# Kernel optimization log

Measured on AMD Instinct MI355X. Metric: run time of the kernel, lower is better.

The kernel has to match this reference:

```python
import jax, jax.numpy as jnp
import numpy as np

N_NODES, N_EDGES, F_DIM, H_DIM = 50000, 800000, 128, 128
BN_EPS = 1e-3  # keras BatchNormalization default epsilon


def setup_inputs() -> dict:
    key = jax.random.key(0)
    k0, k1, k2 = jax.random.split(key, 3)
    edge_pairs = jax.random.randint(k0, (N_EDGES, 2), 0, N_NODES, dtype=jnp.int64 if jax.config.jax_enable_x64 else jnp.int32)
    node_features = jax.random.normal(k1, (N_NODES, F_DIM), dtype=jnp.float32)
    W = jax.random.normal(k2, (F_DIM, H_DIM), dtype=jnp.float32) * (1.0 / np.sqrt(F_DIM))
    b = jnp.zeros((H_DIM,), jnp.float32)
    gamma = jnp.ones((H_DIM,), jnp.float32)
    beta = jnp.zeros((H_DIM,), jnp.float32)
    moving_mean = jnp.zeros((H_DIM,), jnp.float32)
    moving_var = jnp.ones((H_DIM,), jnp.float32)
    return {"edge_pairs": edge_pairs, "node_features": node_features, "W": W, "b": b,
            "gamma": gamma, "beta": beta, "moving_mean": moving_mean, "moving_var": moving_var}


def reference(edge_pairs, node_features, W, b, gamma, beta, moving_mean, moving_var):
    src = edge_pairs[:, 0]
    dst = edge_pairs[:, 1]
    n = node_features.shape[0]

    # linear transform (dropout inactive: training=False)
    t = node_features @ W + b  # [N, H]

    # out-degree by source node
    deg = jax.ops.segment_sum(jnp.ones(src.shape[0], t.dtype), src, num_segments=n)  # [N]
    inv_sqrt_deg = jnp.power(deg, -0.5)  # matches tf.pow(d, -0.5)

    # degree-normalized neighbour messages: d_src^-1/2 * d_dst^-1/2 * t[dst]
    scale = (inv_sqrt_deg[src] * inv_sqrt_deg[dst])[:, None]  # [E,1]
    nb_sum = jax.ops.segment_sum(t[dst] * scale, src, num_segments=n)  # [N, H]

    # source term: segment_mean(deg[src] * t[src]) ; empty segments -> 0 (tf semantics)
    msg = deg[src][:, None] * t[src]  # [E, H]
    seg = jax.ops.segment_sum(msg, src, num_segments=n)  # [N, H]
    src_mean = jnp.where(deg[:, None] > 0, seg / jnp.maximum(deg, 1.0)[:, None], 0.0)

    agg = 0.5 * nb_sum + 0.5 * src_mean

    # batchnorm, inference mode (moving statistics)
    return (agg - moving_mean) * jax.lax.rsqrt(moving_var + BN_EPS) * gamma + beta
```

## Files before the change

kernel.cpp:

```cpp
#include <hip/hip_runtime.h>
#include <math.h>

#define BN_EPS 0.001f
#define CHUNK 2048
#define MAXBUCK 1024

typedef __attribute__((ext_vector_type(8))) short bf16x8;
typedef __attribute__((ext_vector_type(4))) float f32x4;
typedef __attribute__((ext_vector_type(2))) float f32x2;

__device__ inline unsigned bf16rne(float f) {
  unsigned u = __float_as_uint(f);
  return (u + 0x7fffu + ((u >> 16) & 1u)) >> 16;
}

__global__ __launch_bounds__(256) void k_ehist(const int2* __restrict__ ep, int ne,
                                               int nbuck, int* __restrict__ ghist) {
  __shared__ int h[MAXBUCK];
  int c = blockIdx.x, t = threadIdx.x;
  for (int i = t; i < nbuck; i += 256) h[i] = 0;
  __syncthreads();
  int base = c * CHUNK;
  int end = min(base + CHUNK, ne);
  for (int e = base + t; e < end; e += 256) atomicAdd(&h[ep[e].x >> 6], 1);
  __syncthreads();
  int* row = ghist + (size_t)c * nbuck;
  for (int i = t; i < nbuck; i += 256) row[i] = h[i];
}

__global__ __launch_bounds__(512) void k_bscan(int* __restrict__ ghist, int nchunk,
                                               int nbuck, int* __restrict__ btot) {
  __shared__ int s0[512], s1[512];
  int b = blockIdx.x, t = threadIdx.x;
  int v = (t < nchunk) ? ghist[(size_t)t * nbuck + b] : 0;
  s0[t] = v;
  __syncthreads();
  int* src = s0; int* dst = s1;
  for (int off = 1; off < 512; off <<= 1) {
    int x = src[t];
    if (t >= off) x += src[t - off];
    dst[t] = x;
    __syncthreads();
    int* tmp = src; src = dst; dst = tmp;
  }
  if (t < nchunk) ghist[(size_t)t * nbuck + b] = src[t] - v;
  if (t == 0) btot[b] = src[511];
}

__global__ __launch_bounds__(1024) void k_bbase(const int* __restrict__ btot, int nbuck,
                                                int* __restrict__ bbase) {
  __shared__ int s0[1024], s1[1024];
  int t = threadIdx.x;
  int v = (t < nbuck) ? btot[t] : 0;
  s0[t] = v;
  __syncthreads();
  int* src = s0; int* dst = s1;
  for (int off = 1; off < 1024; off <<= 1) {
    int x = src[t];
    if (t >= off) x += src[t - off];
    dst[t] = x;
    __syncthreads();
    int* tmp = src; src = dst; dst = tmp;
  }
  if (t < nbuck) bbase[t] = src[t] - v;
}

__global__ __launch_bounds__(256) void k_ebin(const int2* __restrict__ ep, int ne,
                                              int nbuck, const int* __restrict__ ghist,
                                              const int* __restrict__ bbase,
                                              unsigned* __restrict__ bins) {
  __shared__ int cur[MAXBUCK];
  int c = blockIdx.x, t = threadIdx.x;
  const int* row = ghist + (size_t)c * nbuck;
  for (int i = t; i < nbuck; i += 256) cur[i] = bbase[i] + row[i];
  __syncthreads();
  int base = c * CHUNK;
  int end = min(base + CHUNK, ne);
  for (int e = base + t; e < end; e += 256) {
    int2 p = ep[e];
    int pos = atomicAdd(&cur[p.x >> 6], 1);
    bins[pos] = (unsigned)p.y | ((unsigned)(p.x & 63) << 17);
  }
}

__global__ __launch_bounds__(256) void k_bfinal(const int* __restrict__ bbase,
                                                const int* __restrict__ btot,
                                                const unsigned* __restrict__ bins,
                                                int n, int* __restrict__ deg,
                                                float* __restrict__ isd,
                                                int* __restrict__ offsets,
                                                int* __restrict__ csr_dst) {
  __shared__ int h[64];
  __shared__ int cur[64];
  int bk = blockIdx.x, t = threadIdx.x;
  if (t < 64) h[t] = 0;
  __syncthreads();
  int s = bbase[bk], cnt = btot[bk];
  for (int i = t; i < cnt; i += 256) atomicAdd(&h[bins[s + i] >> 17], 1);
  __syncthreads();
  if (t == 0) {
    int run = s;
    for (int j = 0; j < 64; ++j) { cur[j] = run; run += h[j]; }
  }
  __syncthreads();
  if (t < 64) {
    int node = (bk << 6) + t;
    if (node < n) {
      deg[node] = h[t];
      offsets[node] = cur[t];
      isd[node] = 1.0f / sqrtf((float)h[t]);
    }
  }
  __syncthreads();
  for (int i = t; i < cnt; i += 256) {
    unsigned r = bins[s + i];
    int pos = atomicAdd(&cur[r >> 17], 1);
    csr_dst[pos] = (int)(r & 0x1FFFFu);
  }
}

__global__ __launch_bounds__(256) void k_wsplit(const float* __restrict__ W,
                                                unsigned short* __restrict__ Wh,
                                                unsigned short* __restrict__ Wl) {
  int g = blockIdx.x * 256 + threadIdx.x;
  int frag = g >> 6;
  int lane = g & 63;
  int ct = frag >> 2, ks = frag & 3;
  int col = ct * 16 + (lane & 15);
  int k0 = ks * 32 + (lane >> 4) * 8;
  unsigned short h8[8], l8[8];
#pragma unroll
  for (int j = 0; j < 8; ++j) {
    float x = W[(size_t)(k0 + j) * 128 + col];
    unsigned short h = (unsigned short)(__float_as_uint(x) >> 16);
    float rem = x - __uint_as_float((unsigned)h << 16);
    h8[j] = h;
    l8[j] = (unsigned short)bf16rne(rem);
  }
  *(uint4*)&Wh[(size_t)frag * 512 + lane * 8] = *(uint4*)h8;
  *(uint4*)&Wl[(size_t)frag * 512 + lane * 8] = *(uint4*)l8;
}

__global__ __launch_bounds__(256, 4) void k_gemm(const float* __restrict__ X,
                                                 const unsigned short* __restrict__ Wh,
                                                 const unsigned short* __restrict__ Wl,
                                                 const float* __restrict__ b,
                                                 const float* __restrict__ isd,
                                                 float* __restrict__ T,
                                                 unsigned char* __restrict__ Tb8, int M) {
  int tid = threadIdx.x;
  int wave = tid >> 6, lane = tid & 63;
  int r16 = lane & 15, kq = lane >> 4;
  int ch = wave & 1;
  int rowbase = blockIdx.x * 32 + (wave >> 1) * 16;
  int arow = rowbase + r16;
  bool aok = arow < M;
  const float* xr = X + ((size_t)arow << 7);

  bf16x8 ah[4], al[4];
#pragma unroll
  for (int ks = 0; ks < 4; ++ks) {
    int k0 = ks * 32 + kq * 8;
    float4 v0 = aok ? *(const float4*)(xr + k0) : make_float4(0.f, 0.f, 0.f, 0.f);
    float4 v1 = aok ? *(const float4*)(xr + k0 + 4) : make_float4(0.f, 0.f, 0.f, 0.f);
    float f[8] = {v0.x, v0.y, v0.z, v0.w, v1.x, v1.y, v1.z, v1.w};
    bf16x8 h8, l8;
#pragma unroll
    for (int j = 0; j < 8; ++j) {
      unsigned short h = (unsigned short)(__float_as_uint(f[j]) >> 16);
      float rem = f[j] - __uint_as_float((unsigned)h << 16);
      h8[j] = (short)h;
      l8[j] = (short)bf16rne(rem);
    }
    ah[ks] = h8;
    al[ks] = l8;
  }

  f32x4 acc[4] = {};
#pragma unroll
  for (int ks = 0; ks < 4; ++ks) {
#pragma unroll
    for (int ct = 0; ct < 4; ++ct) {
      int frag = (ch * 4 + ct) * 4 + ks;
      bf16x8 bh = *(const bf16x8*)&Wh[(size_t)frag * 512 + lane * 8];
      bf16x8 bl = *(const bf16x8*)&Wl[(size_t)frag * 512 + lane * 8];
      acc[ct] = __builtin_amdgcn_mfma_f32_16x16x32_bf16(ah[ks], bh, acc[ct], 0, 0, 0);
      acc[ct] = __builtin_amdgcn_mfma_f32_16x16x32_bf16(ah[ks], bl, acc[ct], 0, 0, 0);
      acc[ct] = __builtin_amdgcn_mfma_f32_16x16x32_bf16(al[ks], bh, acc[ct], 0, 0, 0);
    }
  }

  float bias[4];
#pragma unroll
  for (int ct = 0; ct < 4; ++ct) bias[ct] = b[(ch * 4 + ct) * 16 + r16];
  int orow[4];
  float isdr[4];
#pragma unroll
  for (int r = 0; r < 4; ++r) {
    orow[r] = rowbase + kq * 4 + r;
    isdr[r] = (orow[r] < M) ? isd[orow[r]] : 0.f;
  }
#pragma unroll
  for (int ct = 0; ct < 4; ++ct) {
    int col = (ch * 4 + ct) * 16 + r16;
#pragma unroll
    for (int r = 0; r < 4; ++r) {
      float v = acc[ct][r] + bias[ct];
      bool ok = orow[r] < M;
      if (ok) T[((size_t)orow[r] << 7) + col] = v;
      float sv = v * isdr[r];
      float other = __shfl_xor(sv, 1);
      int pk01 = __builtin_amdgcn_cvt_pk_fp8_f32(sv, other, 0, false);
      int pk23 = __shfl_xor(pk01, 2);
      if (ok && (r16 & 3) == 0) {
        unsigned dword = ((unsigned)pk01 & 0xFFFFu) | ((unsigned)pk23 << 16);
        *(unsigned*)&Tb8[((size_t)orow[r] << 7) + (ch * 4 + ct) * 16 + r16] = dword;
      }
    }
  }
}

__global__ __launch_bounds__(256) void k_gather(
    const float* __restrict__ T, const unsigned char* __restrict__ Tb8,
    const int* __restrict__ deg, const float* __restrict__ isd,
    const int* __restrict__ offsets, const int* __restrict__ csr_dst,
    const float* __restrict__ mm, const float* __restrict__ var,
    const float* __restrict__ gamma, const float* __restrict__ beta,
    float* __restrict__ out, int n, int ne) {
  int wave = threadIdx.x >> 6;
  int lane = threadIdx.x & 63;
  int i = blockIdx.x * 4 + wave;
  if (i >= n) return;
  int degi = deg[i];
  int start = offsets[i];
  const unsigned short* rows = (const unsigned short*)Tb8;
  float sx[16] = {}, sy[16] = {};
  for (int e = 0; e < degi; e += 16) {
    int ii = start + e + (lane & 15);
    int dv = (ii < ne) ? csr_dst[ii] : 0;
    unsigned short r[16];
#pragma unroll
    for (int j = 0; j < 16; ++j) {
      int idx = __shfl(dv, j);
      r[j] = rows[((size_t)idx << 6) + lane];
    }
#pragma unroll
    for (int j = 0; j < 16; ++j) {
      int rr = (e + j < degi) ? (int)r[j] : 0;
      f32x2 f = __builtin_amdgcn_cvt_pk_f32_fp8(rr, false);
      sx[j] += f.x;
      sy[j] += f.y;
    }
  }
  float fx = (((sx[0] + sx[1]) + (sx[2] + sx[3])) + ((sx[4] + sx[5]) + (sx[6] + sx[7]))) +
             (((sx[8] + sx[9]) + (sx[10] + sx[11])) + ((sx[12] + sx[13]) + (sx[14] + sx[15])));
  float fy = (((sy[0] + sy[1]) + (sy[2] + sy[3])) + ((sy[4] + sy[5]) + (sy[6] + sy[7]))) +
             (((sy[8] + sy[9]) + (sy[10] + sy[11])) + ((sy[12] + sy[13]) + (sy[14] + sy[15])));
  float aggx = 0.f, aggy = 0.f;
  if (degi > 0) {
    float2 tv = ((const float2*)(T + ((size_t)i << 7)))[lane];
    float isi = isd[i];
    float di = (float)degi;
    aggx = 0.5f * (isi * fx) + 0.5f * (di * tv.x);
    aggy = 0.5f * (isi * fy) + 0.5f * (di * tv.y);
  }
  float2 mmv = ((const float2*)mm)[lane];
  float2 vv = ((const float2*)var)[lane];
  float2 gv = ((const float2*)gamma)[lane];
  float2 bv = ((const float2*)beta)[lane];
  float2 res;
  res.x = (aggx - mmv.x) * rsqrtf(vv.x + BN_EPS) * gv.x + bv.x;
  res.y = (aggy - mmv.y) * rsqrtf(vv.y + BN_EPS) * gv.y + bv.y;
  ((float2*)(out + ((size_t)i << 7)))[lane] = res;
}

static inline size_t align_up(size_t x) { return (x + 255) & ~(size_t)255; }

extern "C" void kernel_launch(void* const* d_in, const int* in_sizes, int n_in,
                              void* d_out, int out_size, void* d_ws, size_t ws_size,
                              hipStream_t stream) {
  const int2* ep = (const int2*)d_in[0];
  const float* X = (const float*)d_in[1];
  const float* W = (const float*)d_in[2];
  const float* b = (const float*)d_in[3];
  const float* gamma = (const float*)d_in[4];
  const float* beta = (const float*)d_in[5];
  const float* mm = (const float*)d_in[6];
  const float* var = (const float*)d_in[7];
  float* out = (float*)d_out;

  const int ne = in_sizes[0] / 2;
  const int n = in_sizes[1] / 128;
  const int nbuck = (n + 63) >> 6;
  const int nchunk = (ne + CHUNK - 1) / CHUNK;

  char* p = (char*)d_ws;
  int* deg = (int*)p;        p += align_up((size_t)n * 4);
  float* isd = (float*)p;    p += align_up((size_t)n * 4);
  int* offsets = (int*)p;    p += align_up((size_t)n * 4);
  int* btot = (int*)p;       p += align_up((size_t)nbuck * 4);
  int* bbase = (int*)p;      p += align_up((size_t)nbuck * 4);
  int* ghist = (int*)p;      p += align_up((size_t)nchunk * nbuck * 4);
  int* csr_dst = (int*)p;    p += align_up((size_t)ne * 4);
  unsigned* bins = (unsigned*)p; p += align_up((size_t)ne * 4);
  unsigned short* Wh = (unsigned short*)p; p += align_up((size_t)128 * 128 * 2);
  unsigned short* Wl = (unsigned short*)p; p += align_up((size_t)128 * 128 * 2);
  float* T = (float*)p;      p += align_up((size_t)n * 128 * 4);
  unsigned char* Tb8 = (unsigned char*)p; p += align_up((size_t)n * 128);

  k_ehist<<<nchunk, 256, 0, stream>>>(ep, ne, nbuck, ghist);
  k_bscan<<<nbuck, 512, 0, stream>>>(ghist, nchunk, nbuck, btot);
  k_bbase<<<1, 1024, 0, stream>>>(btot, nbuck, bbase);
  k_ebin<<<nchunk, 256, 0, stream>>>(ep, ne, nbuck, ghist, bbase, bins);
  k_bfinal<<<nbuck, 256, 0, stream>>>(bbase, btot, bins, n, deg, isd, offsets, csr_dst);
  k_wsplit<<<8, 256, 0, stream>>>(W, Wh, Wl);
  k_gemm<<<(n + 31) / 32, 256, 0, stream>>>(X, Wh, Wl, b, isd, T, Tb8, n);
  k_gather<<<(n + 3) / 4, 256, 0, stream>>>(T, Tb8, deg, isd, offsets, csr_dst,
                                            mm, var, gamma, beta, out, n, ne);
}
```

Baseline: 96.13 us.

## Fuse W bf16 split into GEMM via LDS staging with 1024-thread blocks

Removes the separate k_wsplit launch. Each GEMM block now loads W from global memory, splits it into bf16 hi/lo parts and stores them in LDS in MFMA fragment order. Blocks grow to 1024 threads covering 256 rows, and each wave computes all 128 output columns instead of half. This saves one kernel launch and the global Wh/Wl buffers. In exchange every block redoes the W conversion, uses 64KB of LDS, and runs only 196 blocks, which may limit occupancy.

```diff
diff --git a/kernel.cpp b/kernel.cpp
--- a/kernel.cpp
+++ b/kernel.cpp
@@ -119,40 +119,40 @@
   }
 }
 
-__global__ __launch_bounds__(256) void k_wsplit(const float* __restrict__ W,
-                                                unsigned short* __restrict__ Wh,
-                                                unsigned short* __restrict__ Wl) {
-  int g = blockIdx.x * 256 + threadIdx.x;
-  int frag = g >> 6;
-  int lane = g & 63;
-  int ct = frag >> 2, ks = frag & 3;
-  int col = ct * 16 + (lane & 15);
-  int k0 = ks * 32 + (lane >> 4) * 8;
-  unsigned short h8[8], l8[8];
-#pragma unroll
-  for (int j = 0; j < 8; ++j) {
-    float x = W[(size_t)(k0 + j) * 128 + col];
-    unsigned short h = (unsigned short)(__float_as_uint(x) >> 16);
-    float rem = x - __uint_as_float((unsigned)h << 16);
-    h8[j] = h;
-    l8[j] = (unsigned short)bf16rne(rem);
-  }
-  *(uint4*)&Wh[(size_t)frag * 512 + lane * 8] = *(uint4*)h8;
-  *(uint4*)&Wl[(size_t)frag * 512 + lane * 8] = *(uint4*)l8;
-}
-
-__global__ __launch_bounds__(256, 4) void k_gemm(const float* __restrict__ X,
-                                                 const unsigned short* __restrict__ Wh,
-                                                 const unsigned short* __restrict__ Wl,
-                                                 const float* __restrict__ b,
-                                                 const float* __restrict__ isd,
-                                                 float* __restrict__ T,
-                                                 unsigned char* __restrict__ Tb8, int M) {
+__global__ __launch_bounds__(1024, 4) void k_gemm(const float* __restrict__ X,
+                                                  const float* __restrict__ W,
+                                                  const float* __restrict__ b,
+                                                  const float* __restrict__ isd,
+                                                  float* __restrict__ T,
+                                                  unsigned char* __restrict__ Tb8, int M) {
+  __shared__ unsigned short WhL[16384];
+  __shared__ unsigned short WlL[16384];
   int tid = threadIdx.x;
+
+#pragma unroll
+  for (int it = 0; it < 4; ++it) {
+    int q = tid + it * 1024;
+    int k = q >> 5;
+    int c0 = (q & 31) * 4;
+    float4 v = ((const float4*)W)[q];
+    float vv[4] = {v.x, v.y, v.z, v.w};
+#pragma unroll
+    for (int j2 = 0; j2 < 4; ++j2) {
+      int col = c0 + j2;
+      float x = vv[j2];
+      unsigned short hh = (unsigned short)(__float_as_uint(x) >> 16);
+      float rem = x - __uint_as_float((unsigned)hh << 16);
+      int frag = ((col >> 4) << 2) | (k >> 5);
+      int ln = (((k >> 3) & 3) << 4) | (col & 15);
+      int addr = frag * 512 + ln * 8 + (k & 7);
+      WhL[addr] = hh;
+      WlL[addr] = (unsigned short)bf16rne(rem);
+    }
+  }
+
   int wave = tid >> 6, lane = tid & 63;
   int r16 = lane & 15, kq = lane >> 4;
-  int ch = wave & 1;
-  int rowbase = blockIdx.x * 32 + (wave >> 1) * 16;
+  int rowbase = blockIdx.x * 256 + wave * 16;
   int arow = rowbase + r16;
   bool aok = arow < M;
   const float* xr = X + ((size_t)arow << 7);
@@ -167,32 +167,30 @@
     bf16x8 h8, l8;
 #pragma unroll
     for (int j = 0; j < 8; ++j) {
-      unsigned short h = (unsigned short)(__float_as_uint(f[j]) >> 16);
-      float rem = f[j] - __uint_as_float((unsigned)h << 16);
-      h8[j] = (short)h;
+      unsigned short hh = (unsigned short)(__float_as_uint(f[j]) >> 16);
+      float rem = f[j] - __uint_as_float((unsigned)hh << 16);
+      h8[j] = (short)hh;
       l8[j] = (short)bf16rne(rem);
     }
     ah[ks] = h8;
     al[ks] = l8;
   }
-
-  f32x4 acc[4] = {};
-#pragma unroll
-  for (int ks = 0; ks < 4; ++ks) {
-#pragma unroll
-    for (int ct = 0; ct < 4; ++ct) {
-      int frag = (ch * 4 + ct) * 4 + ks;
-      bf16x8 bh = *(const bf16x8*)&Wh[(size_t)frag * 512 + lane * 8];
-      bf16x8 bl = *(const bf16x8*)&Wl[(size_t)frag * 512 + lane * 8];
+  __syncthreads();
+
+  f32x4 acc[8] = {};
+#pragma unroll
+  for (int ct = 0; ct < 8; ++ct) {
+#pragma unroll
+    for (int ks = 0; ks < 4; ++ks) {
+      int base = (ct * 4 + ks) * 512 + lane * 8;
+      bf16x8 bh = *(const bf16x8*)&WhL[base];
+      bf16x8 bl = *(const bf16x8*)&WlL[base];
       acc[ct] = __builtin_amdgcn_mfma_f32_16x16x32_bf16(ah[ks], bh, acc[ct], 0, 0, 0);
       acc[ct] = __builtin_amdgcn_mfma_f32_16x16x32_bf16(ah[ks], bl, acc[ct], 0, 0, 0);
       acc[ct] = __builtin_amdgcn_mfma_f32_16x16x32_bf16(al[ks], bh, acc[ct], 0, 0, 0);
     }
   }
 
-  float bias[4];
-#pragma unroll
-  for (int ct = 0; ct < 4; ++ct) bias[ct] = b[(ch * 4 + ct) * 16 + r16];
   int orow[4];
   float isdr[4];
 #pragma unroll
@@ -201,11 +199,12 @@
     isdr[r] = (orow[r] < M) ? isd[orow[r]] : 0.f;
   }
 #pragma unroll
-  for (int ct = 0; ct < 4; ++ct) {
-    int col = (ch * 4 + ct) * 16 + r16;
+  for (int ct = 0; ct < 8; ++ct) {
+    int col = ct * 16 + r16;
+    float bias = b[col];
 #pragma unroll
     for (int r = 0; r < 4; ++r) {
-      float v = acc[ct][r] + bias[ct];
+      float v = acc[ct][r] + bias;
       bool ok = orow[r] < M;
       if (ok) T[((size_t)orow[r] << 7) + col] = v;
       float sv = v * isdr[r];
@@ -214,7 +213,7 @@
       int pk23 = __shfl_xor(pk01, 2);
       if (ok && (r16 & 3) == 0) {
         unsigned dword = ((unsigned)pk01 & 0xFFFFu) | ((unsigned)pk23 << 16);
-        *(unsigned*)&Tb8[((size_t)orow[r] << 7) + (ch * 4 + ct) * 16 + r16] = dword;
+        *(unsigned*)&Tb8[((size_t)orow[r] << 7) + ct * 16 + r16] = dword;
       }
     }
   }
@@ -303,8 +302,6 @@
   int* ghist = (int*)p;      p += align_up((size_t)nchunk * nbuck * 4);
   int* csr_dst = (int*)p;    p += align_up((size_t)ne * 4);
   unsigned* bins = (unsigned*)p; p += align_up((size_t)ne * 4);
-  unsigned short* Wh = (unsigned short*)p; p += align_up((size_t)128 * 128 * 2);
-  unsigned short* Wl = (unsigned short*)p; p += align_up((size_t)128 * 128 * 2);
   float* T = (float*)p;      p += align_up((size_t)n * 128 * 4);
   unsigned char* Tb8 = (unsigned char*)p; p += align_up((size_t)n * 128);
 
@@ -313,8 +310,7 @@
   k_bbase<<<1, 1024, 0, stream>>>(btot, nbuck, bbase);
   k_ebin<<<nchunk, 256, 0, stream>>>(ep, ne, nbuck, ghist, bbase, bins);
   k_bfinal<<<nbuck, 256, 0, stream>>>(bbase, btot, bins, n, deg, isd, offsets, csr_dst);
-  k_wsplit<<<8, 256, 0, stream>>>(W, Wh, Wl);
-  k_gemm<<<(n + 31) / 32, 256, 0, stream>>>(X, Wh, Wl, b, isd, T, Tb8, n);
+  k_gemm<<<(n + 255) / 256, 1024, 0, stream>>>(X, W, b, isd, T, Tb8, n);
   k_gather<<<(n + 3) / 4, 256, 0, stream>>>(T, Tb8, deg, isd, offsets, csr_dst,
                                             mm, var, gamma, beta, out, n, ne);
 }
```

Result: faster. 92.49 us (-3.8%).
